# Kernel optimization log

Hardware: AMD Instinct MI355X
Metric: run time of the kernel (lower is better)

The kernel has to match this reference:

```python
import jax, jax.numpy as jnp
import numpy as np

DIM = 192
NUM_HEADS = 6
WS = 8  # window size
N = WS * WS
HEAD_DIM = DIM // NUM_HEADS
SCALE = HEAD_DIM ** -0.5
B_ = 4096  # B * num_windows = 4 * (256/8)^2


def _relative_position_index(ws):
    # Static Swin relative-position index, computed with numpy at trace time.
    coords = np.stack(np.meshgrid(np.arange(ws), np.arange(ws), indexing='ij'))  # (2, ws, ws)
    flat = coords.reshape(2, -1)                       # (2, N)
    rel = flat[:, :, None] - flat[:, None, :]          # (2, N, N)
    rel = rel.transpose(1, 2, 0).astype(np.int64)      # (N, N, 2)
    rel[:, :, 0] += ws - 1
    rel[:, :, 1] += ws - 1
    rel[:, :, 0] *= 2 * ws - 1
    return np.clip(rel.sum(-1), -1000, 1000)           # (N, N)


_REL_IDX = _relative_position_index(WS)


def setup_inputs() -> dict:
    key = jax.random.key(0)
    ks = jax.random.split(key, 6)
    inv = 1.0 / np.sqrt(DIM)
    return {
        'x': jax.random.normal(ks[0], (B_, N, DIM), dtype=jnp.float32),
        'qkv_w': jax.random.normal(ks[1], (3 * DIM, DIM), dtype=jnp.float32) * inv,
        'qkv_b': jax.random.normal(ks[2], (3 * DIM,), dtype=jnp.float32) * 0.02,
        'proj_w': jax.random.normal(ks[3], (DIM, DIM), dtype=jnp.float32) * inv,
        'proj_b': jax.random.normal(ks[4], (DIM,), dtype=jnp.float32) * 0.02,
        'rel_bias_table': jax.random.normal(ks[5], ((2 * WS - 1) ** 2, NUM_HEADS), dtype=jnp.float32) * 0.02,
    }


def reference(x, qkv_w, qkv_b, proj_w, proj_b, rel_bias_table):
    B, n, C = x.shape  # (B_, 64, 192)
    # QKV projection (torch Linear: x @ W^T + b)
    qkv = x @ qkv_w.T + qkv_b                               # (B_, N, 3C)
    qkv = qkv.reshape(B, n, 3, NUM_HEADS, HEAD_DIM)
    qkv = jnp.transpose(qkv, (2, 0, 3, 1, 4))               # (3, B_, h, N, d)
    q, k, v = qkv[0], qkv[1], qkv[2]
    q = q * SCALE
    attn = jnp.einsum('bhnd,bhmd->bhnm', q, k)              # (B_, h, N, N)
    # relative position bias gather: (N*N,) -> (N, N, h) -> (h, N, N)
    bias = rel_bias_table[_REL_IDX.reshape(-1)].reshape(n, n, NUM_HEADS)
    attn = attn + jnp.transpose(bias, (2, 0, 1))[None]
    attn = jax.nn.softmax(attn, axis=-1)
    out = jnp.einsum('bhnm,bhmd->bhnd', attn, v)            # (B_, h, N, d)
    out = jnp.transpose(out, (0, 2, 1, 3)).reshape(B, n, C)
    out = out @ proj_w.T + proj_b
    return out
```

## Files before the change

kernel.cpp:

```cpp
#include <hip/hip_runtime.h>
#include <hip/hip_bf16.h>

#define NWIN 4096
#define NH 6
#define NTOK 64
#define CDIM 192
#define SCALE 0.17677669529663687f

typedef __attribute__((ext_vector_type(8))) short short8;
typedef __attribute__((ext_vector_type(4))) short short4v;
typedef __attribute__((ext_vector_type(4))) float f32x4;

__device__ __forceinline__ short bf(float x) {
  union { __hip_bfloat16 h; short s; } u;
  u.h = __float2bfloat16(x);
  return u.s;
}

__device__ __forceinline__ short8 cvt8v(f32x4 a, f32x4 b) {
  short8 r;
#pragma unroll
  for (int i = 0; i < 4; ++i) { r[i] = bf(a[i]); r[4 + i] = bf(b[i]); }
  return r;
}

__global__ void prep_weights(const float* __restrict__ qkv_w,
                             const float* __restrict__ proj_w,
                             const float* __restrict__ rel_tbl,
                             const float* __restrict__ qkv_b,
                             short* __restrict__ wbuf,
                             float* __restrict__ biasS,
                             float* __restrict__ qkvb2) {
  const int i = blockIdx.x * 256 + threadIdx.x;
  if (i < 110592) {
    float v = qkv_w[i];
    if (i < 36864) v *= SCALE;
    wbuf[i] = bf(v);
  } else if (i < 147456) {
    wbuf[i] = bf(proj_w[i - 110592]);
  } else if (i < 245760) {
    const int j = i - 147456;
    const int h = j >> 12;
    const int n = (j >> 6) & 63;
    const int m = j & 63;
    const int idx = ((n >> 3) - (m >> 3) + 7) * 15 + ((n & 7) - (m & 7) + 7);
    biasS[j] = rel_tbl[idx * NH + h];
  } else {
    const int j = i - 245760;
    if (j < 576) qkvb2[j] = qkv_b[j] * (j < CDIM ? SCALE : 1.0f);
  }
}

__global__ __launch_bounds__(384, 3)
void swin_block_kernel(const float* __restrict__ x,
                       const short* __restrict__ wall,
                       const float* __restrict__ qkvb2,
                       const float* __restrict__ proj_b,
                       const float* __restrict__ biasS,
                       float* __restrict__ out) {
  __shared__ __align__(16) short lds[12288];

  const int b = blockIdx.x;
  const int tid = threadIdx.x;
  const int w = tid >> 6;
  const int lane = tid & 63;
  const int g = lane >> 4;
  const int cc = lane & 15;

  const float* xp = x + (size_t)b * (NTOK * CDIM);

#pragma unroll
  for (int it = 0; it < 2; ++it) {
    const int flat = (tid + it * 384) * 16;
    const int r = flat / CDIM;
    const int c = flat % CDIM;
    const int X = (r & 7) << 3;
    f32x4 a0 = *(const f32x4*)(xp + flat);
    f32x4 a1 = *(const f32x4*)(xp + flat + 4);
    f32x4 a2 = *(const f32x4*)(xp + flat + 8);
    f32x4 a3 = *(const f32x4*)(xp + flat + 12);
    *(short8*)&lds[r * CDIM + (c ^ X)] = cvt8v(a0, a1);
    *(short8*)&lds[r * CDIM + ((c + 8) ^ X)] = cvt8v(a2, a3);
  }
  __syncthreads();

  f32x4 aq_[2][4], ak_[2][4];
#pragma unroll
  for (int ft = 0; ft < 2; ++ft)
#pragma unroll
    for (int mt = 0; mt < 4; ++mt) {
      aq_[ft][mt] = (f32x4){0.f, 0.f, 0.f, 0.f};
      ak_[ft][mt] = (f32x4){0.f, 0.f, 0.f, 0.f};
    }

#pragma unroll 1
  for (int ks = 0; ks < 6; ++ks) {
    short8 afr[4];
#pragma unroll
    for (int mt = 0; mt < 4; ++mt) {
      const int r = mt * 16 + cc;
      afr[mt] = *(const short8*)&lds[r * CDIM + ((ks * 32 + g * 8) ^ ((r & 7) << 3))];
    }
#pragma unroll
    for (int ft = 0; ft < 2; ++ft) {
      const int row = w * 32 + ft * 16 + cc;
      short8 wq8 = *(const short8*)&wall[row * CDIM + ks * 32 + g * 8];
      short8 wk8 = *(const short8*)&wall[(CDIM + row) * CDIM + ks * 32 + g * 8];
#pragma unroll
      for (int mt = 0; mt < 4; ++mt) {
        aq_[ft][mt] = __builtin_amdgcn_mfma_f32_16x16x32_bf16(wq8, afr[mt], aq_[ft][mt], 0, 0, 0);
        ak_[ft][mt] = __builtin_amdgcn_mfma_f32_16x16x32_bf16(wk8, afr[mt], ak_[ft][mt], 0, 0, 0);
      }
    }
  }

  short4v qf[4][2], kf[4][2];
  {
    f32x4 qb[2], kb[2];
#pragma unroll
    for (int ft = 0; ft < 2; ++ft) {
      qb[ft] = *(const f32x4*)&qkvb2[w * 32 + ft * 16 + g * 4];
      kb[ft] = *(const f32x4*)&qkvb2[CDIM + w * 32 + ft * 16 + g * 4];
    }
#pragma unroll
    for (int nt = 0; nt < 4; ++nt)
#pragma unroll
      for (int ft = 0; ft < 2; ++ft)
#pragma unroll
        for (int j = 0; j < 4; ++j) {
          qf[nt][ft][j] = bf(aq_[ft][nt][j] + qb[ft][j]);
          kf[nt][ft][j] = bf(ak_[ft][nt][j] + kb[ft][j]);
        }
  }

  f32x4 av_[4][2];
#pragma unroll
  for (int mt = 0; mt < 4; ++mt)
#pragma unroll
    for (int dt = 0; dt < 2; ++dt)
      av_[mt][dt] = (f32x4){0.f, 0.f, 0.f, 0.f};

#pragma unroll 1
  for (int ks = 0; ks < 6; ++ks) {
    short8 afr[4];
#pragma unroll
    for (int mt = 0; mt < 4; ++mt) {
      const int r = mt * 16 + cc;
      afr[mt] = *(const short8*)&lds[r * CDIM + ((ks * 32 + g * 8) ^ ((r & 7) << 3))];
    }
#pragma unroll
    for (int dt = 0; dt < 2; ++dt) {
      short8 wv8 = *(const short8*)&wall[(2 * CDIM + w * 32 + dt * 16 + cc) * CDIM + ks * 32 + g * 8];
#pragma unroll
      for (int mt = 0; mt < 4; ++mt)
        av_[mt][dt] = __builtin_amdgcn_mfma_f32_16x16x32_bf16(afr[mt], wv8, av_[mt][dt], 0, 0, 0);
    }
  }

  short4v vf[2][4];
  {
    float vb[2];
    vb[0] = qkvb2[2 * CDIM + w * 32 + cc];
    vb[1] = qkvb2[2 * CDIM + w * 32 + 16 + cc];
#pragma unroll
    for (int dt = 0; dt < 2; ++dt)
#pragma unroll
      for (int kt = 0; kt < 4; ++kt)
#pragma unroll
        for (int j = 0; j < 4; ++j)
          vf[dt][kt][j] = bf(av_[kt][dt][j] + vb[dt]);
  }

  __syncthreads();

  const float* bs = biasS + w * 4096;
#pragma unroll
  for (int qh = 0; qh < 2; ++qh) {
    f32x4 sacc[4][2];
#pragma unroll
    for (int mt = 0; mt < 4; ++mt)
#pragma unroll
      for (int nl = 0; nl < 2; ++nl) {
        const int n = qh * 32 + nl * 16 + cc;
        f32x4 z = *(const f32x4*)&bs[n * 64 + mt * 16 + g * 4];
        z = __builtin_amdgcn_mfma_f32_16x16x16bf16_1k(kf[mt][0], qf[qh * 2 + nl][0], z, 0, 0, 0);
        sacc[mt][nl] = __builtin_amdgcn_mfma_f32_16x16x16bf16_1k(kf[mt][1], qf[qh * 2 + nl][1], z, 0, 0, 0);
      }

    short4v pf[2][4];
#pragma unroll
    for (int nl = 0; nl < 2; ++nl) {
      float sum = 0.f;
#pragma unroll
      for (int mt = 0; mt < 4; ++mt)
#pragma unroll
        for (int e = 0; e < 4; ++e) {
          float p = __expf(sacc[mt][nl][e]);
          sacc[mt][nl][e] = p;
          sum += p;
        }
      sum += __shfl_xor(sum, 16);
      sum += __shfl_xor(sum, 32);
      const float rinv = __builtin_amdgcn_rcpf(sum);
#pragma unroll
      for (int kt = 0; kt < 4; ++kt)
#pragma unroll
        for (int j = 0; j < 4; ++j)
          pf[nl][kt][j] = bf(sacc[kt][nl][j] * rinv);
    }

    f32x4 oacc[2][2];
#pragma unroll
    for (int nl = 0; nl < 2; ++nl)
#pragma unroll
      for (int dt = 0; dt < 2; ++dt) {
        f32x4 z = (f32x4){0.f, 0.f, 0.f, 0.f};
#pragma unroll
        for (int kt = 0; kt < 4; ++kt)
          z = __builtin_amdgcn_mfma_f32_16x16x16bf16_1k(pf[nl][kt], vf[dt][kt], z, 0, 0, 0);
        oacc[nl][dt] = z;
      }

#pragma unroll
    for (int nl = 0; nl < 2; ++nl)
#pragma unroll
      for (int dt = 0; dt < 2; ++dt)
#pragma unroll
        for (int e = 0; e < 4; ++e) {
          const int r = qh * 32 + nl * 16 + g * 4 + e;
          const int c = w * 32 + dt * 16 + cc;
          lds[r * CDIM + (c ^ ((r & 7) << 3))] = bf(oacc[nl][dt][e]);
        }
  }
  __syncthreads();

  f32x4 pacc[4][2];
#pragma unroll
  for (int mt = 0; mt < 4; ++mt)
#pragma unroll
    for (int jt = 0; jt < 2; ++jt)
      pacc[mt][jt] = (f32x4){0.f, 0.f, 0.f, 0.f};

#pragma unroll 1
  for (int ks = 0; ks < 6; ++ks) {
    short8 afr[4];
#pragma unroll
    for (int mt = 0; mt < 4; ++mt) {
      const int r = mt * 16 + cc;
      afr[mt] = *(const short8*)&lds[r * CDIM + ((ks * 32 + g * 8) ^ ((r & 7) << 3))];
    }
#pragma unroll
    for (int jt = 0; jt < 2; ++jt) {
      const int j = w * 32 + jt * 16 + cc;
      short8 wfr = *(const short8*)&wall[(3 * CDIM + j) * CDIM + ks * 32 + g * 8];
#pragma unroll
      for (int mt = 0; mt < 4; ++mt)
        pacc[mt][jt] = __builtin_amdgcn_mfma_f32_16x16x32_bf16(afr[mt], wfr, pacc[mt][jt], 0, 0, 0);
    }
  }

  float* op = out + (size_t)b * (NTOK * CDIM);
#pragma unroll
  for (int jt = 0; jt < 2; ++jt) {
    const int j = w * 32 + jt * 16 + cc;
    const float pb = proj_b[j];
#pragma unroll
    for (int mt = 0; mt < 4; ++mt)
#pragma unroll
      for (int e = 0; e < 4; ++e)
        op[(mt * 16 + g * 4 + e) * CDIM + j] = pacc[mt][jt][e] + pb;
  }
}

extern "C" void kernel_launch(void* const* d_in, const int* in_sizes, int n_in,
                              void* d_out, int out_size, void* d_ws, size_t ws_size,
                              hipStream_t stream) {
  const float* x       = (const float*)d_in[0];
  const float* qkv_w   = (const float*)d_in[1];
  const float* qkv_b   = (const float*)d_in[2];
  const float* proj_w  = (const float*)d_in[3];
  const float* proj_b  = (const float*)d_in[4];
  const float* rel_tbl = (const float*)d_in[5];
  float* out = (float*)d_out;

  short* wbuf  = (short*)d_ws;
  float* biasS = (float*)(wbuf + 147456);
  float* qkvb2 = biasS + 98304;

  prep_weights<<<963, 256, 0, stream>>>(qkv_w, proj_w, rel_tbl, qkv_b,
                                        wbuf, biasS, qkvb2);
  swin_block_kernel<<<NWIN, 384, 0, stream>>>(x, wbuf, qkvb2, proj_b, biasS, out);
}
```

Measured before the change: 262.3 us.

## Prefetch weight fragments, fold log2e into softmax, vectorize bias and output

The three GEMM k-loops now software-pipeline their weight fragment loads from global memory one step ahead, and the first fragments are issued before the barrier so they overlap the x staging. Log2(e) is folded into the Q scale, Q bias and relative bias so the softmax can use exp2. The bias table is re-laid out to match the per-lane MFMA accumulator order, giving each lane one contiguous read. The projection is transposed (weights as the A operand) so output stores become 16-byte vector stores. The cost is more live registers under launch_bounds(384,3), which could cause spills.

```diff
diff --git a/kernel.cpp b/kernel.cpp
--- a/kernel.cpp
+++ b/kernel.cpp
@@ -6,10 +6,14 @@
 #define NTOK 64
 #define CDIM 192
 #define SCALE 0.17677669529663687f
+#define LOG2E 1.4426950408889634f
 
 typedef __attribute__((ext_vector_type(8))) short short8;
 typedef __attribute__((ext_vector_type(4))) short short4v;
 typedef __attribute__((ext_vector_type(4))) float f32x4;
+
+#define MFMA32(A, B, C) __builtin_amdgcn_mfma_f32_16x16x32_bf16(A, B, C, 0, 0, 0)
+#define MFMA16(A, B, C) __builtin_amdgcn_mfma_f32_16x16x16bf16_1k(A, B, C, 0, 0, 0)
 
 __device__ __forceinline__ short bf(float x) {
   union { __hip_bfloat16 h; short s; } u;
@@ -34,22 +38,57 @@
   const int i = blockIdx.x * 256 + threadIdx.x;
   if (i < 110592) {
     float v = qkv_w[i];
-    if (i < 36864) v *= SCALE;
+    if (i < 36864) v *= SCALE * LOG2E;
     wbuf[i] = bf(v);
   } else if (i < 147456) {
     wbuf[i] = bf(proj_w[i - 110592]);
   } else if (i < 245760) {
     const int j = i - 147456;
-    const int h = j >> 12;
-    const int n = (j >> 6) & 63;
-    const int m = j & 63;
+    const int h = j >> 14;
+    const int t = j & 16383;
+    const int slot = t >> 10;
+    const int ln = (t >> 2) & 63;
+    const int e = t & 3;
+    const int qh = slot >> 3, nl = (slot >> 2) & 1, mt = slot & 3;
+    const int n = qh * 32 + nl * 16 + (ln & 15);
+    const int m = mt * 16 + (ln >> 4) * 4 + e;
     const int idx = ((n >> 3) - (m >> 3) + 7) * 15 + ((n & 7) - (m & 7) + 7);
-    biasS[j] = rel_tbl[idx * NH + h];
+    biasS[j] = rel_tbl[idx * NH + h] * LOG2E;
   } else {
     const int j = i - 245760;
-    if (j < 576) qkvb2[j] = qkv_b[j] * (j < CDIM ? SCALE : 1.0f);
-  }
-}
+    if (j < 576) qkvb2[j] = qkv_b[j] * (j < CDIM ? SCALE * LOG2E : 1.0f);
+  }
+}
+
+#define LDAF(dst, kc) do {                                              \
+  _Pragma("unroll")                                                     \
+  for (int mt_ = 0; mt_ < 4; ++mt_) {                                   \
+    const int r_ = mt_ * 16 + cc;                                       \
+    dst[mt_] = *(const short8*)&lds[r_ * CDIM + ((kc) ^ ((r_ & 7) << 3))]; \
+  } } while (0)
+
+#define MMQK(q0, q1, k0, k1, af) do {                                   \
+  _Pragma("unroll")                                                     \
+  for (int mt_ = 0; mt_ < 4; ++mt_) {                                   \
+    aq_[0][mt_] = MFMA32(q0, af[mt_], aq_[0][mt_]);                     \
+    aq_[1][mt_] = MFMA32(q1, af[mt_], aq_[1][mt_]);                     \
+    ak_[0][mt_] = MFMA32(k0, af[mt_], ak_[0][mt_]);                     \
+    ak_[1][mt_] = MFMA32(k1, af[mt_], ak_[1][mt_]);                     \
+  } } while (0)
+
+#define MMV(v0, v1, af) do {                                            \
+  _Pragma("unroll")                                                     \
+  for (int mt_ = 0; mt_ < 4; ++mt_) {                                   \
+    av_[mt_][0] = MFMA32(af[mt_], v0, av_[mt_][0]);                     \
+    av_[mt_][1] = MFMA32(af[mt_], v1, av_[mt_][1]);                     \
+  } } while (0)
+
+#define MMP(f0, f1, af) do {                                            \
+  _Pragma("unroll")                                                     \
+  for (int mt_ = 0; mt_ < 4; ++mt_) {                                   \
+    pacc[mt_][0] = MFMA32(f0, af[mt_], pacc[mt_][0]);                   \
+    pacc[mt_][1] = MFMA32(f1, af[mt_], pacc[mt_][1]);                   \
+  } } while (0)
 
 __global__ __launch_bounds__(384, 3)
 void swin_block_kernel(const float* __restrict__ x,
@@ -68,6 +107,12 @@
   const int cc = lane & 15;
 
   const float* xp = x + (size_t)b * (NTOK * CDIM);
+
+  const int rq0 = (w * 32 + cc) * CDIM;
+  const int rq1 = rq0 + 16 * CDIM;
+  const short* wk_ = wall + CDIM * CDIM;
+  const short* wv_ = wall + 2 * CDIM * CDIM;
+  const short* wp_ = wall + 3 * CDIM * CDIM;
 
 #pragma unroll
   for (int it = 0; it < 2; ++it) {
@@ -82,6 +127,11 @@
     *(short8*)&lds[r * CDIM + (c ^ X)] = cvt8v(a0, a1);
     *(short8*)&lds[r * CDIM + ((c + 8) ^ X)] = cvt8v(a2, a3);
   }
+
+  short8 qA0 = *(const short8*)&wall[rq0 + g * 8];
+  short8 qA1 = *(const short8*)&wall[rq1 + g * 8];
+  short8 kA0 = *(const short8*)&wk_[rq0 + g * 8];
+  short8 kA1 = *(const short8*)&wk_[rq1 + g * 8];
   __syncthreads();
 
   f32x4 aq_[2][4], ak_[2][4];
@@ -94,24 +144,25 @@
     }
 
 #pragma unroll 1
-  for (int ks = 0; ks < 6; ++ks) {
-    short8 afr[4];
-#pragma unroll
-    for (int mt = 0; mt < 4; ++mt) {
-      const int r = mt * 16 + cc;
-      afr[mt] = *(const short8*)&lds[r * CDIM + ((ks * 32 + g * 8) ^ ((r & 7) << 3))];
-    }
-#pragma unroll
-    for (int ft = 0; ft < 2; ++ft) {
-      const int row = w * 32 + ft * 16 + cc;
-      short8 wq8 = *(const short8*)&wall[row * CDIM + ks * 32 + g * 8];
-      short8 wk8 = *(const short8*)&wall[(CDIM + row) * CDIM + ks * 32 + g * 8];
-#pragma unroll
-      for (int mt = 0; mt < 4; ++mt) {
-        aq_[ft][mt] = __builtin_amdgcn_mfma_f32_16x16x32_bf16(wq8, afr[mt], aq_[ft][mt], 0, 0, 0);
-        ak_[ft][mt] = __builtin_amdgcn_mfma_f32_16x16x32_bf16(wk8, afr[mt], ak_[ft][mt], 0, 0, 0);
-      }
-    }
+  for (int ks = 0; ks < 6; ks += 2) {
+    const int c1 = (ks + 1) * 32 + g * 8;
+    short8 qB0 = *(const short8*)&wall[rq0 + c1];
+    short8 qB1 = *(const short8*)&wall[rq1 + c1];
+    short8 kB0 = *(const short8*)&wk_[rq0 + c1];
+    short8 kB1 = *(const short8*)&wk_[rq1 + c1];
+    short8 af0[4];
+    LDAF(af0, ks * 32 + g * 8);
+    MMQK(qA0, qA1, kA0, kA1, af0);
+    if (ks < 4) {
+      const int c2 = (ks + 2) * 32 + g * 8;
+      qA0 = *(const short8*)&wall[rq0 + c2];
+      qA1 = *(const short8*)&wall[rq1 + c2];
+      kA0 = *(const short8*)&wk_[rq0 + c2];
+      kA1 = *(const short8*)&wk_[rq1 + c2];
+    }
+    short8 af1[4];
+    LDAF(af1, c1);
+    MMQK(qB0, qB1, kB0, kB1, af1);
   }
 
   short4v qf[4][2], kf[4][2];
@@ -140,21 +191,24 @@
     for (int dt = 0; dt < 2; ++dt)
       av_[mt][dt] = (f32x4){0.f, 0.f, 0.f, 0.f};
 
+  short8 vA0 = *(const short8*)&wv_[rq0 + g * 8];
+  short8 vA1 = *(const short8*)&wv_[rq1 + g * 8];
 #pragma unroll 1
-  for (int ks = 0; ks < 6; ++ks) {
-    short8 afr[4];
-#pragma unroll
-    for (int mt = 0; mt < 4; ++mt) {
-      const int r = mt * 16 + cc;
-      afr[mt] = *(const short8*)&lds[r * CDIM + ((ks * 32 + g * 8) ^ ((r & 7) << 3))];
-    }
-#pragma unroll
-    for (int dt = 0; dt < 2; ++dt) {
-      short8 wv8 = *(const short8*)&wall[(2 * CDIM + w * 32 + dt * 16 + cc) * CDIM + ks * 32 + g * 8];
-#pragma unroll
-      for (int mt = 0; mt < 4; ++mt)
-        av_[mt][dt] = __builtin_amdgcn_mfma_f32_16x16x32_bf16(afr[mt], wv8, av_[mt][dt], 0, 0, 0);
-    }
+  for (int ks = 0; ks < 6; ks += 2) {
+    const int c1 = (ks + 1) * 32 + g * 8;
+    short8 vB0 = *(const short8*)&wv_[rq0 + c1];
+    short8 vB1 = *(const short8*)&wv_[rq1 + c1];
+    short8 af0[4];
+    LDAF(af0, ks * 32 + g * 8);
+    MMV(vA0, vA1, af0);
+    if (ks < 4) {
+      const int c2 = (ks + 2) * 32 + g * 8;
+      vA0 = *(const short8*)&wv_[rq0 + c2];
+      vA1 = *(const short8*)&wv_[rq1 + c2];
+    }
+    short8 af1[4];
+    LDAF(af1, c1);
+    MMV(vB0, vB1, af1);
   }
 
   short4v vf[2][4];
@@ -173,7 +227,7 @@
 
   __syncthreads();
 
-  const float* bs = biasS + w * 4096;
+  const float* bs = biasS + w * 16384;
 #pragma unroll
   for (int qh = 0; qh < 2; ++qh) {
     f32x4 sacc[4][2];
@@ -181,10 +235,9 @@
     for (int mt = 0; mt < 4; ++mt)
 #pragma unroll
       for (int nl = 0; nl < 2; ++nl) {
-        const int n = qh * 32 + nl * 16 + cc;
-        f32x4 z = *(const f32x4*)&bs[n * 64 + mt * 16 + g * 4];
-        z = __builtin_amdgcn_mfma_f32_16x16x16bf16_1k(kf[mt][0], qf[qh * 2 + nl][0], z, 0, 0, 0);
-        sacc[mt][nl] = __builtin_amdgcn_mfma_f32_16x16x16bf16_1k(kf[mt][1], qf[qh * 2 + nl][1], z, 0, 0, 0);
+        f32x4 z = *(const f32x4*)&bs[(((qh * 2 + nl) << 2) + mt) * 1024 + lane * 4];
+        z = MFMA16(kf[mt][0], qf[qh * 2 + nl][0], z);
+        sacc[mt][nl] = MFMA16(kf[mt][1], qf[qh * 2 + nl][1], z);
       }
 
     short4v pf[2][4];
@@ -195,7 +248,7 @@
       for (int mt = 0; mt < 4; ++mt)
 #pragma unroll
         for (int e = 0; e < 4; ++e) {
-          float p = __expf(sacc[mt][nl][e]);
+          float p = exp2f(sacc[mt][nl][e]);
           sacc[mt][nl][e] = p;
           sum += p;
         }
@@ -217,7 +270,7 @@
         f32x4 z = (f32x4){0.f, 0.f, 0.f, 0.f};
 #pragma unroll
         for (int kt = 0; kt < 4; ++kt)
-          z = __builtin_amdgcn_mfma_f32_16x16x16bf16_1k(pf[nl][kt], vf[dt][kt], z, 0, 0, 0);
+          z = MFMA16(pf[nl][kt], vf[dt][kt], z);
         oacc[nl][dt] = z;
       }
 
@@ -232,6 +285,9 @@
           lds[r * CDIM + (c ^ ((r & 7) << 3))] = bf(oacc[nl][dt][e]);
         }
   }
+
+  short8 pA0 = *(const short8*)&wp_[rq0 + g * 8];
+  short8 pA1 = *(const short8*)&wp_[rq1 + g * 8];
   __syncthreads();
 
   f32x4 pacc[4][2];
@@ -242,34 +298,34 @@
       pacc[mt][jt] = (f32x4){0.f, 0.f, 0.f, 0.f};
 
 #pragma unroll 1
-  for (int ks = 0; ks < 6; ++ks) {
-    short8 afr[4];
-#pragma unroll
-    for (int mt = 0; mt < 4; ++mt) {
-      const int r = mt * 16 + cc;
-      afr[mt] = *(const short8*)&lds[r * CDIM + ((ks * 32 + g * 8) ^ ((r & 7) << 3))];
-    }
+  for (int ks = 0; ks < 6; ks += 2) {
+    const int c1 = (ks + 1) * 32 + g * 8;
+    short8 pB0 = *(const short8*)&wp_[rq0 + c1];
+    short8 pB1 = *(const short8*)&wp_[rq1 + c1];
+    short8 af0[4];
+    LDAF(af0, ks * 32 + g * 8);
+    MMP(pA0, pA1, af0);
+    if (ks < 4) {
+      const int c2 = (ks + 2) * 32 + g * 8;
+      pA0 = *(const short8*)&wp_[rq0 + c2];
+      pA1 = *(const short8*)&wp_[rq1 + c2];
+    }
+    short8 af1[4];
+    LDAF(af1, c1);
+    MMP(pB0, pB1, af1);
+  }
+
+  float* op = out + (size_t)b * (NTOK * CDIM);
+  f32x4 pbv[2];
+  pbv[0] = *(const f32x4*)&proj_b[w * 32 + g * 4];
+  pbv[1] = *(const f32x4*)&proj_b[w * 32 + 16 + g * 4];
+#pragma unroll
+  for (int mt = 0; mt < 4; ++mt)
 #pragma unroll
     for (int jt = 0; jt < 2; ++jt) {
-      const int j = w * 32 + jt * 16 + cc;
-      short8 wfr = *(const short8*)&wall[(3 * CDIM + j) * CDIM + ks * 32 + g * 8];
-#pragma unroll
-      for (int mt = 0; mt < 4; ++mt)
-        pacc[mt][jt] = __builtin_amdgcn_mfma_f32_16x16x32_bf16(afr[mt], wfr, pacc[mt][jt], 0, 0, 0);
-    }
-  }
-
-  float* op = out + (size_t)b * (NTOK * CDIM);
-#pragma unroll
-  for (int jt = 0; jt < 2; ++jt) {
-    const int j = w * 32 + jt * 16 + cc;
-    const float pb = proj_b[j];
-#pragma unroll
-    for (int mt = 0; mt < 4; ++mt)
-#pragma unroll
-      for (int e = 0; e < 4; ++e)
-        op[(mt * 16 + g * 4 + e) * CDIM + j] = pacc[mt][jt][e] + pb;
-  }
+      f32x4 v = pacc[mt][jt] + pbv[jt];
+      *(f32x4*)&op[(mt * 16 + cc) * CDIM + w * 32 + jt * 16 + g * 4] = v;
+    }
 }
 
 extern "C" void kernel_launch(void* const* d_in, const int* in_sizes, int n_in,
```

Measured after the change: 268.3 us. 2.3% more time.

## Split QKV GEMMs, prelayout bias per lane, fold log2e, vectorize output stores

Applied to the files above, without the earlier changes.

Splits the fused Q/K projection loop into separate Q, K and V passes to cut live accumulator registers. The relative-position bias is pre-laid out in MFMA fragment order so each lane reads it contiguously. log2(e) is folded into the Q weights, Q bias and position bias so softmax can use exp2 directly. The projection GEMM is transposed so each lane writes its output as float4 vector stores instead of scalar strided stores. The cost is that activation tiles are now read from LDS three times during the Q, K and V passes instead of twice.

```diff
diff --git a/kernel.cpp b/kernel.cpp
--- a/kernel.cpp
+++ b/kernel.cpp
@@ -6,10 +6,14 @@
 #define NTOK 64
 #define CDIM 192
 #define SCALE 0.17677669529663687f
+#define LOG2E 1.4426950408889634f
 
 typedef __attribute__((ext_vector_type(8))) short short8;
 typedef __attribute__((ext_vector_type(4))) short short4v;
 typedef __attribute__((ext_vector_type(4))) float f32x4;
+
+#define MFMA32(A, B, C) __builtin_amdgcn_mfma_f32_16x16x32_bf16(A, B, C, 0, 0, 0)
+#define MFMA16(A, B, C) __builtin_amdgcn_mfma_f32_16x16x16bf16_1k(A, B, C, 0, 0, 0)
 
 __device__ __forceinline__ short bf(float x) {
   union { __hip_bfloat16 h; short s; } u;
@@ -34,22 +38,34 @@
   const int i = blockIdx.x * 256 + threadIdx.x;
   if (i < 110592) {
     float v = qkv_w[i];
-    if (i < 36864) v *= SCALE;
+    if (i < 36864) v *= SCALE * LOG2E;
     wbuf[i] = bf(v);
   } else if (i < 147456) {
     wbuf[i] = bf(proj_w[i - 110592]);
   } else if (i < 245760) {
     const int j = i - 147456;
-    const int h = j >> 12;
-    const int n = (j >> 6) & 63;
-    const int m = j & 63;
+    const int h = j >> 14;
+    const int t = j & 16383;
+    const int slot = t >> 10;
+    const int ln = (t >> 2) & 63;
+    const int e = t & 3;
+    const int qh = slot >> 3, nl = (slot >> 2) & 1, mt = slot & 3;
+    const int n = qh * 32 + nl * 16 + (ln & 15);
+    const int m = mt * 16 + (ln >> 4) * 4 + e;
     const int idx = ((n >> 3) - (m >> 3) + 7) * 15 + ((n & 7) - (m & 7) + 7);
-    biasS[j] = rel_tbl[idx * NH + h];
+    biasS[j] = rel_tbl[idx * NH + h] * LOG2E;
   } else {
     const int j = i - 245760;
-    if (j < 576) qkvb2[j] = qkv_b[j] * (j < CDIM ? SCALE : 1.0f);
-  }
-}
+    if (j < 576) qkvb2[j] = qkv_b[j] * (j < CDIM ? SCALE * LOG2E : 1.0f);
+  }
+}
+
+#define LDAF(dst, kc) do {                                              \
+  _Pragma("unroll")                                                     \
+  for (int mt_ = 0; mt_ < 4; ++mt_) {                                   \
+    const int r_ = mt_ * 16 + cc;                                       \
+    dst[mt_] = *(const short8*)&lds[r_ * CDIM + ((kc) ^ ((r_ & 7) << 3))]; \
+  } } while (0)
 
 __global__ __launch_bounds__(384, 3)
 void swin_block_kernel(const float* __restrict__ x,
@@ -68,6 +84,12 @@
   const int cc = lane & 15;
 
   const float* xp = x + (size_t)b * (NTOK * CDIM);
+
+  const int rq0 = (w * 32 + cc) * CDIM;
+  const int rq1 = rq0 + 16 * CDIM;
+  const short* wk_ = wall + CDIM * CDIM;
+  const short* wv_ = wall + 2 * CDIM * CDIM;
+  const short* wp_ = wall + 3 * CDIM * CDIM;
 
 #pragma unroll
   for (int it = 0; it < 2; ++it) {
@@ -84,96 +106,105 @@
   }
   __syncthreads();
 
-  f32x4 aq_[2][4], ak_[2][4];
-#pragma unroll
-  for (int ft = 0; ft < 2; ++ft)
-#pragma unroll
-    for (int mt = 0; mt < 4; ++mt) {
-      aq_[ft][mt] = (f32x4){0.f, 0.f, 0.f, 0.f};
-      ak_[ft][mt] = (f32x4){0.f, 0.f, 0.f, 0.f};
-    }
-
+  short4v qf[4][2], kf[4][2];
+  short4v vf[2][4];
+
+  {
+    f32x4 acc[2][4];
+#pragma unroll
+    for (int ft = 0; ft < 2; ++ft)
+#pragma unroll
+      for (int mt = 0; mt < 4; ++mt)
+        acc[ft][mt] = (f32x4){0.f, 0.f, 0.f, 0.f};
 #pragma unroll 1
-  for (int ks = 0; ks < 6; ++ks) {
-    short8 afr[4];
-#pragma unroll
-    for (int mt = 0; mt < 4; ++mt) {
-      const int r = mt * 16 + cc;
-      afr[mt] = *(const short8*)&lds[r * CDIM + ((ks * 32 + g * 8) ^ ((r & 7) << 3))];
+    for (int ks = 0; ks < 6; ++ks) {
+      const int c0 = ks * 32 + g * 8;
+      short8 w0 = *(const short8*)&wall[rq0 + c0];
+      short8 w1 = *(const short8*)&wall[rq1 + c0];
+      short8 afr[4];
+      LDAF(afr, c0);
+#pragma unroll
+      for (int mt = 0; mt < 4; ++mt) {
+        acc[0][mt] = MFMA32(w0, afr[mt], acc[0][mt]);
+        acc[1][mt] = MFMA32(w1, afr[mt], acc[1][mt]);
+      }
     }
 #pragma unroll
     for (int ft = 0; ft < 2; ++ft) {
-      const int row = w * 32 + ft * 16 + cc;
-      short8 wq8 = *(const short8*)&wall[row * CDIM + ks * 32 + g * 8];
-      short8 wk8 = *(const short8*)&wall[(CDIM + row) * CDIM + ks * 32 + g * 8];
+      f32x4 qb = *(const f32x4*)&qkvb2[w * 32 + ft * 16 + g * 4];
+#pragma unroll
+      for (int nt = 0; nt < 4; ++nt)
+#pragma unroll
+        for (int j = 0; j < 4; ++j)
+          qf[nt][ft][j] = bf(acc[ft][nt][j] + qb[j]);
+    }
+  }
+
+  {
+    f32x4 acc[2][4];
+#pragma unroll
+    for (int ft = 0; ft < 2; ++ft)
+#pragma unroll
+      for (int mt = 0; mt < 4; ++mt)
+        acc[ft][mt] = (f32x4){0.f, 0.f, 0.f, 0.f};
+#pragma unroll 1
+    for (int ks = 0; ks < 6; ++ks) {
+      const int c0 = ks * 32 + g * 8;
+      short8 w0 = *(const short8*)&wk_[rq0 + c0];
+      short8 w1 = *(const short8*)&wk_[rq1 + c0];
+      short8 afr[4];
+      LDAF(afr, c0);
 #pragma unroll
       for (int mt = 0; mt < 4; ++mt) {
-        aq_[ft][mt] = __builtin_amdgcn_mfma_f32_16x16x32_bf16(wq8, afr[mt], aq_[ft][mt], 0, 0, 0);
-        ak_[ft][mt] = __builtin_amdgcn_mfma_f32_16x16x32_bf16(wk8, afr[mt], ak_[ft][mt], 0, 0, 0);
-      }
-    }
-  }
-
-  short4v qf[4][2], kf[4][2];
+        acc[0][mt] = MFMA32(w0, afr[mt], acc[0][mt]);
+        acc[1][mt] = MFMA32(w1, afr[mt], acc[1][mt]);
+      }
+    }
+#pragma unroll
+    for (int ft = 0; ft < 2; ++ft) {
+      f32x4 kb = *(const f32x4*)&qkvb2[CDIM + w * 32 + ft * 16 + g * 4];
+#pragma unroll
+      for (int nt = 0; nt < 4; ++nt)
+#pragma unroll
+        for (int j = 0; j < 4; ++j)
+          kf[nt][ft][j] = bf(acc[ft][nt][j] + kb[j]);
+    }
+  }
+
   {
-    f32x4 qb[2], kb[2];
-#pragma unroll
-    for (int ft = 0; ft < 2; ++ft) {
-      qb[ft] = *(const f32x4*)&qkvb2[w * 32 + ft * 16 + g * 4];
-      kb[ft] = *(const f32x4*)&qkvb2[CDIM + w * 32 + ft * 16 + g * 4];
-    }
-#pragma unroll
-    for (int nt = 0; nt < 4; ++nt)
-#pragma unroll
-      for (int ft = 0; ft < 2; ++ft)
-#pragma unroll
-        for (int j = 0; j < 4; ++j) {
-          qf[nt][ft][j] = bf(aq_[ft][nt][j] + qb[ft][j]);
-          kf[nt][ft][j] = bf(ak_[ft][nt][j] + kb[ft][j]);
-        }
-  }
-
-  f32x4 av_[4][2];
-#pragma unroll
-  for (int mt = 0; mt < 4; ++mt)
-#pragma unroll
-    for (int dt = 0; dt < 2; ++dt)
-      av_[mt][dt] = (f32x4){0.f, 0.f, 0.f, 0.f};
-
+    f32x4 acc[4][2];
+#pragma unroll
+    for (int mt = 0; mt < 4; ++mt)
+#pragma unroll
+      for (int dt = 0; dt < 2; ++dt)
+        acc[mt][dt] = (f32x4){0.f, 0.f, 0.f, 0.f};
 #pragma unroll 1
-  for (int ks = 0; ks < 6; ++ks) {
-    short8 afr[4];
-#pragma unroll
-    for (int mt = 0; mt < 4; ++mt) {
-      const int r = mt * 16 + cc;
-      afr[mt] = *(const short8*)&lds[r * CDIM + ((ks * 32 + g * 8) ^ ((r & 7) << 3))];
-    }
-#pragma unroll
-    for (int dt = 0; dt < 2; ++dt) {
-      short8 wv8 = *(const short8*)&wall[(2 * CDIM + w * 32 + dt * 16 + cc) * CDIM + ks * 32 + g * 8];
-#pragma unroll
-      for (int mt = 0; mt < 4; ++mt)
-        av_[mt][dt] = __builtin_amdgcn_mfma_f32_16x16x32_bf16(afr[mt], wv8, av_[mt][dt], 0, 0, 0);
-    }
-  }
-
-  short4v vf[2][4];
-  {
-    float vb[2];
-    vb[0] = qkvb2[2 * CDIM + w * 32 + cc];
-    vb[1] = qkvb2[2 * CDIM + w * 32 + 16 + cc];
-#pragma unroll
-    for (int dt = 0; dt < 2; ++dt)
-#pragma unroll
-      for (int kt = 0; kt < 4; ++kt)
-#pragma unroll
-        for (int j = 0; j < 4; ++j)
-          vf[dt][kt][j] = bf(av_[kt][dt][j] + vb[dt]);
+    for (int ks = 0; ks < 6; ++ks) {
+      const int c0 = ks * 32 + g * 8;
+      short8 w0 = *(const short8*)&wv_[rq0 + c0];
+      short8 w1 = *(const short8*)&wv_[rq1 + c0];
+      short8 afr[4];
+      LDAF(afr, c0);
+#pragma unroll
+      for (int mt = 0; mt < 4; ++mt) {
+        acc[mt][0] = MFMA32(afr[mt], w0, acc[mt][0]);
+        acc[mt][1] = MFMA32(afr[mt], w1, acc[mt][1]);
+      }
+    }
+    float vb0 = qkvb2[2 * CDIM + w * 32 + cc];
+    float vb1 = qkvb2[2 * CDIM + w * 32 + 16 + cc];
+#pragma unroll
+    for (int kt = 0; kt < 4; ++kt)
+#pragma unroll
+      for (int j = 0; j < 4; ++j) {
+        vf[0][kt][j] = bf(acc[kt][0][j] + vb0);
+        vf[1][kt][j] = bf(acc[kt][1][j] + vb1);
+      }
   }
 
   __syncthreads();
 
-  const float* bs = biasS + w * 4096;
+  const float* bs = biasS + w * 16384;
 #pragma unroll
   for (int qh = 0; qh < 2; ++qh) {
     f32x4 sacc[4][2];
@@ -181,10 +212,9 @@
     for (int mt = 0; mt < 4; ++mt)
 #pragma unroll
       for (int nl = 0; nl < 2; ++nl) {
-        const int n = qh * 32 + nl * 16 + cc;
-        f32x4 z = *(const f32x4*)&bs[n * 64 + mt * 16 + g * 4];
-        z = __builtin_amdgcn_mfma_f32_16x16x16bf16_1k(kf[mt][0], qf[qh * 2 + nl][0], z, 0, 0, 0);
-        sacc[mt][nl] = __builtin_amdgcn_mfma_f32_16x16x16bf16_1k(kf[mt][1], qf[qh * 2 + nl][1], z, 0, 0, 0);
+        f32x4 z = *(const f32x4*)&bs[(((qh * 2 + nl) << 2) + mt) * 1024 + lane * 4];
+        z = MFMA16(kf[mt][0], qf[qh * 2 + nl][0], z);
+        sacc[mt][nl] = MFMA16(kf[mt][1], qf[qh * 2 + nl][1], z);
       }
 
     short4v pf[2][4];
@@ -195,7 +225,7 @@
       for (int mt = 0; mt < 4; ++mt)
 #pragma unroll
         for (int e = 0; e < 4; ++e) {
-          float p = __expf(sacc[mt][nl][e]);
+          float p = exp2f(sacc[mt][nl][e]);
           sacc[mt][nl][e] = p;
           sum += p;
         }
@@ -217,7 +247,7 @@
         f32x4 z = (f32x4){0.f, 0.f, 0.f, 0.f};
 #pragma unroll
         for (int kt = 0; kt < 4; ++kt)
-          z = __builtin_amdgcn_mfma_f32_16x16x16bf16_1k(pf[nl][kt], vf[dt][kt], z, 0, 0, 0);
+          z = MFMA16(pf[nl][kt], vf[dt][kt], z);
         oacc[nl][dt] = z;
       }
 
@@ -243,33 +273,29 @@
 
 #pragma unroll 1
   for (int ks = 0; ks < 6; ++ks) {
+    const int c0 = ks * 32 + g * 8;
+    short8 p0 = *(const short8*)&wp_[rq0 + c0];
+    short8 p1 = *(const short8*)&wp_[rq1 + c0];
     short8 afr[4];
+    LDAF(afr, c0);
 #pragma unroll
     for (int mt = 0; mt < 4; ++mt) {
-      const int r = mt * 16 + cc;
-      afr[mt] = *(const short8*)&lds[r * CDIM + ((ks * 32 + g * 8) ^ ((r & 7) << 3))];
-    }
+      pacc[mt][0] = MFMA32(p0, afr[mt], pacc[mt][0]);
+      pacc[mt][1] = MFMA32(p1, afr[mt], pacc[mt][1]);
+    }
+  }
+
+  float* op = out + (size_t)b * (NTOK * CDIM);
+  f32x4 pbv[2];
+  pbv[0] = *(const f32x4*)&proj_b[w * 32 + g * 4];
+  pbv[1] = *(const f32x4*)&proj_b[w * 32 + 16 + g * 4];
+#pragma unroll
+  for (int mt = 0; mt < 4; ++mt)
 #pragma unroll
     for (int jt = 0; jt < 2; ++jt) {
-      const int j = w * 32 + jt * 16 + cc;
-      short8 wfr = *(const short8*)&wall[(3 * CDIM + j) * CDIM + ks * 32 + g * 8];
-#pragma unroll
-      for (int mt = 0; mt < 4; ++mt)
-        pacc[mt][jt] = __builtin_amdgcn_mfma_f32_16x16x32_bf16(afr[mt], wfr, pacc[mt][jt], 0, 0, 0);
-    }
-  }
-
-  float* op = out + (size_t)b * (NTOK * CDIM);
-#pragma unroll
-  for (int jt = 0; jt < 2; ++jt) {
-    const int j = w * 32 + jt * 16 + cc;
-    const float pb = proj_b[j];
-#pragma unroll
-    for (int mt = 0; mt < 4; ++mt)
-#pragma unroll
-      for (int e = 0; e < 4; ++e)
-        op[(mt * 16 + g * 4 + e) * CDIM + j] = pacc[mt][jt][e] + pb;
-  }
+      f32x4 v = pacc[mt][jt] + pbv[jt];
+      *(f32x4*)&op[(mt * 16 + cc) * CDIM + w * 32 + jt * 16 + g * 4] = v;
+    }
 }
 
 extern "C" void kernel_launch(void* const* d_in, const int* in_sizes, int n_in,
```

Measured after the change: 274.7 us. +4.7%, slower.

## Process two windows per block and prefetch the second window's input

Applied to the files above, without the earlier changes.

Each block now handles two windows sequentially, with LDS doubled to hold a second input tile. The second window's x tile is loaded and converted into LDS during the first window's QKV phase, so the global load overlaps compute. The grid is halved, which amortizes block setup. The larger LDS footprint (48KB) and the loop structure may reduce occupancy and leave fewer blocks to balance across CUs.

```diff
diff --git a/kernel.cpp b/kernel.cpp
--- a/kernel.cpp
+++ b/kernel.cpp
@@ -10,6 +10,9 @@
 typedef __attribute__((ext_vector_type(8))) short short8;
 typedef __attribute__((ext_vector_type(4))) short short4v;
 typedef __attribute__((ext_vector_type(4))) float f32x4;
+
+#define MFMA32(A, B, C) __builtin_amdgcn_mfma_f32_16x16x32_bf16(A, B, C, 0, 0, 0)
+#define MFMA16(A, B, C) __builtin_amdgcn_mfma_f32_16x16x16bf16_1k(A, B, C, 0, 0, 0)
 
 __device__ __forceinline__ short bf(float x) {
   union { __hip_bfloat16 h; short s; } u;
@@ -51,24 +54,14 @@
   }
 }
 
-__global__ __launch_bounds__(384, 3)
-void swin_block_kernel(const float* __restrict__ x,
-                       const short* __restrict__ wall,
-                       const float* __restrict__ qkvb2,
-                       const float* __restrict__ proj_b,
-                       const float* __restrict__ biasS,
-                       float* __restrict__ out) {
-  __shared__ __align__(16) short lds[12288];
-
-  const int b = blockIdx.x;
-  const int tid = threadIdx.x;
-  const int w = tid >> 6;
-  const int lane = tid & 63;
-  const int g = lane >> 4;
-  const int cc = lane & 15;
-
-  const float* xp = x + (size_t)b * (NTOK * CDIM);
-
+#define LDAF(base, dst, kc) do {                                        \
+  _Pragma("unroll")                                                     \
+  for (int mt_ = 0; mt_ < 4; ++mt_) {                                   \
+    const int r_ = mt_ * 16 + cc;                                       \
+    dst[mt_] = *(const short8*)&(base)[r_ * CDIM + ((kc) ^ ((r_ & 7) << 3))]; \
+  } } while (0)
+
+__device__ __forceinline__ void stage0(short* dstT, const float* xp, int tid) {
 #pragma unroll
   for (int it = 0; it < 2; ++it) {
     const int flat = (tid + it * 384) * 16;
@@ -79,196 +72,211 @@
     f32x4 a1 = *(const f32x4*)(xp + flat + 4);
     f32x4 a2 = *(const f32x4*)(xp + flat + 8);
     f32x4 a3 = *(const f32x4*)(xp + flat + 12);
-    *(short8*)&lds[r * CDIM + (c ^ X)] = cvt8v(a0, a1);
-    *(short8*)&lds[r * CDIM + ((c + 8) ^ X)] = cvt8v(a2, a3);
+    *(short8*)&dstT[r * CDIM + (c ^ X)] = cvt8v(a0, a1);
+    *(short8*)&dstT[r * CDIM + ((c + 8) ^ X)] = cvt8v(a2, a3);
   }
+}
+
+__global__ __launch_bounds__(384, 3)
+void swin_block_kernel(const float* __restrict__ x,
+                       const short* __restrict__ wall,
+                       const float* __restrict__ qkvb2,
+                       const float* __restrict__ proj_b,
+                       const float* __restrict__ biasS,
+                       float* __restrict__ out) {
+  __shared__ __align__(16) short lds[24576];
+
+  const int b = blockIdx.x;
+  const int tid = threadIdx.x;
+  const int w = tid >> 6;
+  const int lane = tid & 63;
+  const int g = lane >> 4;
+  const int cc = lane & 15;
+
+  const int rq0 = (w * 32 + cc) * CDIM;
+  const int rq1 = rq0 + 16 * CDIM;
+  const short* wk_ = wall + CDIM * CDIM;
+  const short* wv_ = wall + 2 * CDIM * CDIM;
+  const short* wp_ = wall + 3 * CDIM * CDIM;
+
+  stage0(lds, x + (size_t)(b * 2) * (NTOK * CDIM), tid);
   __syncthreads();
 
-  f32x4 aq_[2][4], ak_[2][4];
-#pragma unroll
-  for (int ft = 0; ft < 2; ++ft)
-#pragma unroll
-    for (int mt = 0; mt < 4; ++mt) {
-      aq_[ft][mt] = (f32x4){0.f, 0.f, 0.f, 0.f};
-      ak_[ft][mt] = (f32x4){0.f, 0.f, 0.f, 0.f};
-    }
-
 #pragma unroll 1
-  for (int ks = 0; ks < 6; ++ks) {
-    short8 afr[4];
-#pragma unroll
-    for (int mt = 0; mt < 4; ++mt) {
-      const int r = mt * 16 + cc;
-      afr[mt] = *(const short8*)&lds[r * CDIM + ((ks * 32 + g * 8) ^ ((r & 7) << 3))];
-    }
-#pragma unroll
-    for (int ft = 0; ft < 2; ++ft) {
-      const int row = w * 32 + ft * 16 + cc;
-      short8 wq8 = *(const short8*)&wall[row * CDIM + ks * 32 + g * 8];
-      short8 wk8 = *(const short8*)&wall[(CDIM + row) * CDIM + ks * 32 + g * 8];
+  for (int wi = 0; wi < 2; ++wi) {
+    short* const XT = lds + wi * 12288;
+
+    short4v qf[4][2], kf[4][2];
+    {
+      f32x4 aq_[2][4], ak_[2][4];
+#pragma unroll
+      for (int ft = 0; ft < 2; ++ft)
+#pragma unroll
+        for (int mt = 0; mt < 4; ++mt) {
+          aq_[ft][mt] = (f32x4){0.f, 0.f, 0.f, 0.f};
+          ak_[ft][mt] = (f32x4){0.f, 0.f, 0.f, 0.f};
+        }
+#pragma unroll 1
+      for (int ks = 0; ks < 6; ++ks) {
+        const int c0 = ks * 32 + g * 8;
+        short8 wq8 = *(const short8*)&wall[rq0 + c0];
+        short8 wq9 = *(const short8*)&wall[rq1 + c0];
+        short8 wk8 = *(const short8*)&wk_[rq0 + c0];
+        short8 wk9 = *(const short8*)&wk_[rq1 + c0];
+        short8 afr[4];
+        LDAF(XT, afr, c0);
+#pragma unroll
+        for (int mt = 0; mt < 4; ++mt) {
+          aq_[0][mt] = MFMA32(wq8, afr[mt], aq_[0][mt]);
+          aq_[1][mt] = MFMA32(wq9, afr[mt], aq_[1][mt]);
+          ak_[0][mt] = MFMA32(wk8, afr[mt], ak_[0][mt]);
+          ak_[1][mt] = MFMA32(wk9, afr[mt], ak_[1][mt]);
+        }
+      }
+#pragma unroll
+      for (int ft = 0; ft < 2; ++ft) {
+        f32x4 qb = *(const f32x4*)&qkvb2[w * 32 + ft * 16 + g * 4];
+        f32x4 kb = *(const f32x4*)&qkvb2[CDIM + w * 32 + ft * 16 + g * 4];
+#pragma unroll
+        for (int nt = 0; nt < 4; ++nt)
+#pragma unroll
+          for (int j = 0; j < 4; ++j) {
+            qf[nt][ft][j] = bf(aq_[ft][nt][j] + qb[j]);
+            kf[nt][ft][j] = bf(ak_[ft][nt][j] + kb[j]);
+          }
+      }
+    }
+
+    short4v vf[2][4];
+    {
+      f32x4 av_[4][2];
+#pragma unroll
+      for (int mt = 0; mt < 4; ++mt)
+#pragma unroll
+        for (int dt = 0; dt < 2; ++dt)
+          av_[mt][dt] = (f32x4){0.f, 0.f, 0.f, 0.f};
+#pragma unroll 1
+      for (int ks = 0; ks < 6; ++ks) {
+        const int c0 = ks * 32 + g * 8;
+        short8 wv8 = *(const short8*)&wv_[rq0 + c0];
+        short8 wv9 = *(const short8*)&wv_[rq1 + c0];
+        short8 afr[4];
+        LDAF(XT, afr, c0);
+#pragma unroll
+        for (int mt = 0; mt < 4; ++mt) {
+          av_[mt][0] = MFMA32(afr[mt], wv8, av_[mt][0]);
+          av_[mt][1] = MFMA32(afr[mt], wv9, av_[mt][1]);
+        }
+      }
+      float vb0 = qkvb2[2 * CDIM + w * 32 + cc];
+      float vb1 = qkvb2[2 * CDIM + w * 32 + 16 + cc];
+#pragma unroll
+      for (int kt = 0; kt < 4; ++kt)
+#pragma unroll
+        for (int j = 0; j < 4; ++j) {
+          vf[0][kt][j] = bf(av_[kt][0][j] + vb0);
+          vf[1][kt][j] = bf(av_[kt][1][j] + vb1);
+        }
+    }
+
+    if (wi == 0)
+      stage0(lds + 12288, x + (size_t)(b * 2 + 1) * (NTOK * CDIM), tid);
+
+    __syncthreads();
+
+    const float* bs = biasS + w * 4096;
+#pragma unroll
+    for (int qh = 0; qh < 2; ++qh) {
+      f32x4 sacc[4][2];
+#pragma unroll
+      for (int mt = 0; mt < 4; ++mt)
+#pragma unroll
+        for (int nl = 0; nl < 2; ++nl) {
+          const int n = qh * 32 + nl * 16 + cc;
+          f32x4 z = *(const f32x4*)&bs[n * 64 + mt * 16 + g * 4];
+          z = MFMA16(kf[mt][0], qf[qh * 2 + nl][0], z);
+          sacc[mt][nl] = MFMA16(kf[mt][1], qf[qh * 2 + nl][1], z);
+        }
+
+      short4v pf[2][4];
+#pragma unroll
+      for (int nl = 0; nl < 2; ++nl) {
+        float sum = 0.f;
+#pragma unroll
+        for (int mt = 0; mt < 4; ++mt)
+#pragma unroll
+          for (int e = 0; e < 4; ++e) {
+            float p = __expf(sacc[mt][nl][e]);
+            sacc[mt][nl][e] = p;
+            sum += p;
+          }
+        sum += __shfl_xor(sum, 16);
+        sum += __shfl_xor(sum, 32);
+        const float rinv = __builtin_amdgcn_rcpf(sum);
+#pragma unroll
+        for (int kt = 0; kt < 4; ++kt)
+#pragma unroll
+          for (int j = 0; j < 4; ++j)
+            pf[nl][kt][j] = bf(sacc[kt][nl][j] * rinv);
+      }
+
+      f32x4 oacc[2][2];
+#pragma unroll
+      for (int nl = 0; nl < 2; ++nl)
+#pragma unroll
+        for (int dt = 0; dt < 2; ++dt) {
+          f32x4 z = (f32x4){0.f, 0.f, 0.f, 0.f};
+#pragma unroll
+          for (int kt = 0; kt < 4; ++kt)
+            z = MFMA16(pf[nl][kt], vf[dt][kt], z);
+          oacc[nl][dt] = z;
+        }
+
+#pragma unroll
+      for (int nl = 0; nl < 2; ++nl)
+#pragma unroll
+        for (int dt = 0; dt < 2; ++dt)
+#pragma unroll
+          for (int e = 0; e < 4; ++e) {
+            const int r = qh * 32 + nl * 16 + g * 4 + e;
+            const int c = w * 32 + dt * 16 + cc;
+            XT[r * CDIM + (c ^ ((r & 7) << 3))] = bf(oacc[nl][dt][e]);
+          }
+    }
+    __syncthreads();
+
+    f32x4 pacc[4][2];
+#pragma unroll
+    for (int mt = 0; mt < 4; ++mt)
+#pragma unroll
+      for (int jt = 0; jt < 2; ++jt)
+        pacc[mt][jt] = (f32x4){0.f, 0.f, 0.f, 0.f};
+
+#pragma unroll 1
+    for (int ks = 0; ks < 6; ++ks) {
+      const int c0 = ks * 32 + g * 8;
+      short8 p0 = *(const short8*)&wp_[rq0 + c0];
+      short8 p1 = *(const short8*)&wp_[rq1 + c0];
+      short8 afr[4];
+      LDAF(XT, afr, c0);
 #pragma unroll
       for (int mt = 0; mt < 4; ++mt) {
-        aq_[ft][mt] = __builtin_amdgcn_mfma_f32_16x16x32_bf16(wq8, afr[mt], aq_[ft][mt], 0, 0, 0);
-        ak_[ft][mt] = __builtin_amdgcn_mfma_f32_16x16x32_bf16(wk8, afr[mt], ak_[ft][mt], 0, 0, 0);
-      }
-    }
-  }
-
-  short4v qf[4][2], kf[4][2];
-  {
-    f32x4 qb[2], kb[2];
-#pragma unroll
-    for (int ft = 0; ft < 2; ++ft) {
-      qb[ft] = *(const f32x4*)&qkvb2[w * 32 + ft * 16 + g * 4];
-      kb[ft] = *(const f32x4*)&qkvb2[CDIM + w * 32 + ft * 16 + g * 4];
-    }
-#pragma unroll
-    for (int nt = 0; nt < 4; ++nt)
-#pragma unroll
-      for (int ft = 0; ft < 2; ++ft)
-#pragma unroll
-        for (int j = 0; j < 4; ++j) {
-          qf[nt][ft][j] = bf(aq_[ft][nt][j] + qb[ft][j]);
-          kf[nt][ft][j] = bf(ak_[ft][nt][j] + kb[ft][j]);
-        }
-  }
-
-  f32x4 av_[4][2];
-#pragma unroll
-  for (int mt = 0; mt < 4; ++mt)
-#pragma unroll
-    for (int dt = 0; dt < 2; ++dt)
-      av_[mt][dt] = (f32x4){0.f, 0.f, 0.f, 0.f};
-
-#pragma unroll 1
-  for (int ks = 0; ks < 6; ++ks) {
-    short8 afr[4];
-#pragma unroll
-    for (int mt = 0; mt < 4; ++mt) {
-      const int r = mt * 16 + cc;
-      afr[mt] = *(const short8*)&lds[r * CDIM + ((ks * 32 + g * 8) ^ ((r & 7) << 3))];
-    }
-#pragma unroll
-    for (int dt = 0; dt < 2; ++dt) {
-      short8 wv8 = *(const short8*)&wall[(2 * CDIM + w * 32 + dt * 16 + cc) * CDIM + ks * 32 + g * 8];
-#pragma unroll
-      for (int mt = 0; mt < 4; ++mt)
-        av_[mt][dt] = __builtin_amdgcn_mfma_f32_16x16x32_bf16(afr[mt], wv8, av_[mt][dt], 0, 0, 0);
-    }
-  }
-
-  short4v vf[2][4];
-  {
-    float vb[2];
-    vb[0] = qkvb2[2 * CDIM + w * 32 + cc];
-    vb[1] = qkvb2[2 * CDIM + w * 32 + 16 + cc];
-#pragma unroll
-    for (int dt = 0; dt < 2; ++dt)
-#pragma unroll
-      for (int kt = 0; kt < 4; ++kt)
-#pragma unroll
-        for (int j = 0; j < 4; ++j)
-          vf[dt][kt][j] = bf(av_[kt][dt][j] + vb[dt]);
-  }
-
-  __syncthreads();
-
-  const float* bs = biasS + w * 4096;
-#pragma unroll
-  for (int qh = 0; qh < 2; ++qh) {
-    f32x4 sacc[4][2];
-#pragma unroll
-    for (int mt = 0; mt < 4; ++mt)
-#pragma unroll
-      for (int nl = 0; nl < 2; ++nl) {
-        const int n = qh * 32 + nl * 16 + cc;
-        f32x4 z = *(const f32x4*)&bs[n * 64 + mt * 16 + g * 4];
-        z = __builtin_amdgcn_mfma_f32_16x16x16bf16_1k(kf[mt][0], qf[qh * 2 + nl][0], z, 0, 0, 0);
-        sacc[mt][nl] = __builtin_amdgcn_mfma_f32_16x16x16bf16_1k(kf[mt][1], qf[qh * 2 + nl][1], z, 0, 0, 0);
-      }
-
-    short4v pf[2][4];
-#pragma unroll
-    for (int nl = 0; nl < 2; ++nl) {
-      float sum = 0.f;
-#pragma unroll
-      for (int mt = 0; mt < 4; ++mt)
-#pragma unroll
-        for (int e = 0; e < 4; ++e) {
-          float p = __expf(sacc[mt][nl][e]);
-          sacc[mt][nl][e] = p;
-          sum += p;
-        }
-      sum += __shfl_xor(sum, 16);
-      sum += __shfl_xor(sum, 32);
-      const float rinv = __builtin_amdgcn_rcpf(sum);
-#pragma unroll
-      for (int kt = 0; kt < 4; ++kt)
-#pragma unroll
-        for (int j = 0; j < 4; ++j)
-          pf[nl][kt][j] = bf(sacc[kt][nl][j] * rinv);
-    }
-
-    f32x4 oacc[2][2];
-#pragma unroll
-    for (int nl = 0; nl < 2; ++nl)
-#pragma unroll
-      for (int dt = 0; dt < 2; ++dt) {
-        f32x4 z = (f32x4){0.f, 0.f, 0.f, 0.f};
-#pragma unroll
-        for (int kt = 0; kt < 4; ++kt)
-          z = __builtin_amdgcn_mfma_f32_16x16x16bf16_1k(pf[nl][kt], vf[dt][kt], z, 0, 0, 0);
-        oacc[nl][dt] = z;
-      }
-
-#pragma unroll
-    for (int nl = 0; nl < 2; ++nl)
-#pragma unroll
-      for (int dt = 0; dt < 2; ++dt)
-#pragma unroll
-        for (int e = 0; e < 4; ++e) {
-          const int r = qh * 32 + nl * 16 + g * 4 + e;
-          const int c = w * 32 + dt * 16 + cc;
-          lds[r * CDIM + (c ^ ((r & 7) << 3))] = bf(oacc[nl][dt][e]);
-        }
-  }
-  __syncthreads();
-
-  f32x4 pacc[4][2];
-#pragma unroll
-  for (int mt = 0; mt < 4; ++mt)
-#pragma unroll
-    for (int jt = 0; jt < 2; ++jt)
-      pacc[mt][jt] = (f32x4){0.f, 0.f, 0.f, 0.f};
-
-#pragma unroll 1
-  for (int ks = 0; ks < 6; ++ks) {
-    short8 afr[4];
-#pragma unroll
-    for (int mt = 0; mt < 4; ++mt) {
-      const int r = mt * 16 + cc;
-      afr[mt] = *(const short8*)&lds[r * CDIM + ((ks * 32 + g * 8) ^ ((r & 7) << 3))];
-    }
+        pacc[mt][0] = MFMA32(afr[mt], p0, pacc[mt][0]);
+        pacc[mt][1] = MFMA32(afr[mt], p1, pacc[mt][1]);
+      }
+    }
+
+    float* op = out + (size_t)(b * 2 + wi) * (NTOK * CDIM);
 #pragma unroll
     for (int jt = 0; jt < 2; ++jt) {
       const int j = w * 32 + jt * 16 + cc;
-      short8 wfr = *(const short8*)&wall[(3 * CDIM + j) * CDIM + ks * 32 + g * 8];
+      const float pb = proj_b[j];
 #pragma unroll
       for (int mt = 0; mt < 4; ++mt)
-        pacc[mt][jt] = __builtin_amdgcn_mfma_f32_16x16x32_bf16(afr[mt], wfr, pacc[mt][jt], 0, 0, 0);
-    }
-  }
-
-  float* op = out + (size_t)b * (NTOK * CDIM);
-#pragma unroll
-  for (int jt = 0; jt < 2; ++jt) {
-    const int j = w * 32 + jt * 16 + cc;
-    const float pb = proj_b[j];
-#pragma unroll
-    for (int mt = 0; mt < 4; ++mt)
-#pragma unroll
-      for (int e = 0; e < 4; ++e)
-        op[(mt * 16 + g * 4 + e) * CDIM + j] = pacc[mt][jt][e] + pb;
+#pragma unroll
+        for (int e = 0; e < 4; ++e)
+          op[(mt * 16 + g * 4 + e) * CDIM + j] = pacc[mt][jt][e] + pb;
+    }
   }
 }
 
@@ -289,5 +297,6 @@
 
   prep_weights<<<963, 256, 0, stream>>>(qkv_w, proj_w, rel_tbl, qkv_b,
                                         wbuf, biasS, qkvb2);
-  swin_block_kernel<<<NWIN, 384, 0, stream>>>(x, wbuf, qkvb2, proj_b, biasS, out);
-}
+  swin_block_kernel<<<NWIN / 2, 384, 0, stream>>>(x, wbuf, qkvb2, proj_b,
+                                                  biasS, out);
+}
```

After: 485.9 us. 85.2% more time.
